# Kernel optimization log

Measured on AMD Instinct MI355X. Metric: run time of the kernel, lower is better.

Reference implementation:

```python
import jax, jax.numpy as jnp
import numpy as np

B, S, D, H, K = 2, 2048, 1024, 16, 64


def setup_inputs() -> dict:
    key = jax.random.key(0)
    k1, k2, k3 = jax.random.split(key, 3)
    x = jax.random.normal(k1, (B, S, D), dtype=jnp.float32)
    # causal mask: 1 where query can attend to key (key_pos <= pos)
    mask = jnp.tril(jnp.ones((S, S), dtype=jnp.float32))
    W_qkv = jax.random.normal(k2, (D, 3, H, K), dtype=jnp.float32) * 0.02
    b_qkv = jnp.zeros((3, H, K), dtype=jnp.float32)
    W_proj = jax.random.normal(k3, (H, K, D), dtype=jnp.float32) * 0.02
    b_proj = jnp.zeros((D,), dtype=jnp.float32)
    return {"x": x, "mask": mask, "W_qkv": W_qkv, "b_qkv": b_qkv,
            "W_proj": W_proj, "b_proj": b_proj, "layer_idx": 0}


def reference(x, mask, W_qkv, b_qkv, W_proj, b_proj, layer_idx):
    # c_attn: [B,S,D] @ [D,3,H,K] -> [B,S,3,H,K]
    qkv = jnp.einsum('bsd,dthk->bsthk', x, W_qkv) + b_qkv
    q, k, v = qkv[:, :, 0], qkv[:, :, 1], qkv[:, :, 2]  # each [B,S,H,K]
    scale = jax.lax.rsqrt(float(K))  # scale_attn_by_inverse_layer_idx=False
    q = q * scale
    # attn scores over key_size: [B,H,S(pos),S(key_pos)]
    scores = jnp.einsum('bshk,bthk->bhst', q, k)
    scores = scores + (1.0 - mask) * -1e9
    weights = jax.nn.softmax(scores, axis=-1).astype(x.dtype)
    # attn_pdrop = 0.0 -> dropout is identity
    attn_out = jnp.einsum('bhst,bthk->bshk', weights, v)  # [B,S,H,K]
    out = jnp.einsum('bshk,hkd->bsd', attn_out, W_proj) + b_proj
    return out
```

## Files before the change

### kernel.cpp

```cpp
#include <hip/hip_runtime.h>

typedef __bf16 bf16x8 __attribute__((ext_vector_type(8)));
typedef float f32x4 __attribute__((ext_vector_type(4)));
typedef float f32x16 __attribute__((ext_vector_type(16)));
typedef unsigned short u16x8 __attribute__((ext_vector_type(8)));

constexpr int S_LEN = 2048;
constexpr int QKV1  = 2 * 16 * 2048 * 64;

__device__ inline unsigned short f2bf(float f) {
    __bf16 h = (__bf16)f;
    return __builtin_bit_cast(unsigned short, h);
}

__device__ inline void gll16(const void* g, void* l) {
    __builtin_amdgcn_global_load_lds(
        (const __attribute__((address_space(1))) unsigned int*)g,
        (__attribute__((address_space(3))) unsigned int*)l,
        16, 0, 0);
}

__global__ __launch_bounds__(256) void cvt_f32_bf16(
    const float* __restrict__ src, unsigned short* __restrict__ dst, int n4)
{
    int i = blockIdx.x * 256 + threadIdx.x;
    if (i >= n4) return;
    float4 v = ((const float4*)src)[i];
    ushort4 u;
    u.x = f2bf(v.x); u.y = f2bf(v.y); u.z = f2bf(v.z); u.w = f2bf(v.w);
    ((ushort4*)dst)[i] = u;
}

__global__ __launch_bounds__(256) void transpose_cvt(
    const float* __restrict__ src, unsigned short* __restrict__ dst, int R, int C)
{
    __shared__ float t[32][33];
    const int c0 = blockIdx.x * 32, r0 = blockIdx.y * 32;
    const int tx = threadIdx.x, ty = threadIdx.y;
    #pragma unroll
    for (int i = 0; i < 4; ++i)
        t[ty * 4 + i][tx] = src[(size_t)(r0 + ty * 4 + i) * C + c0 + tx];
    __syncthreads();
    #pragma unroll
    for (int i = 0; i < 4; ++i)
        dst[(size_t)(c0 + ty * 4 + i) * R + r0 + tx] = f2bf(t[tx][ty * 4 + i]);
}

template<int EPI>
__global__ __launch_bounds__(256) void gemm128(
    const unsigned short* __restrict__ A,
    const unsigned short* __restrict__ Bt,
    const float* __restrict__ bias,
    void* __restrict__ outp, int M, int N, int K)
{
    __shared__ unsigned short As[2][128 * 32];
    __shared__ unsigned short Bs[2][128 * 32];
    const int tid = threadIdx.x, lane = tid & 63, wid = tid >> 6;
    const int q = lane & 15, g = lane >> 4;
    const int wr = wid >> 1, wc = wid & 1;

    const int nbx = N >> 7;
    const int cpx = gridDim.x >> 3;
    const int bid = blockIdx.x;
    const int swz = (bid & 7) * cpx + (bid >> 3);
    const int m0 = (swz / nbx) * 128, n0 = (swz % nbx) * 128;

    const int srow_in = lane >> 2;
    const int sslot   = (lane & 3) ^ (srow_in & 3);
    auto stage = [&](int buf, int k0) {
        #pragma unroll
        for (int i = 0; i < 2; ++i) {
            int c = wid * 2 + i;
            int row = c * 16 + srow_in;
            gll16(&A [(size_t)(m0 + row) * K + k0 + sslot * 8], &As[buf][c * 512]);
            gll16(&Bt[(size_t)(n0 + row) * K + k0 + sslot * 8], &Bs[buf][c * 512]);
        }
    };

    f32x4 acc[4][4];
    #pragma unroll
    for (int i = 0; i < 4; ++i)
        #pragma unroll
        for (int j = 0; j < 4; ++j) acc[i][j] = (f32x4){0.f, 0.f, 0.f, 0.f};

    const int NSTEP = K >> 5;
    const int rslot = (g ^ (q & 3)) * 8;
    stage(0, 0);
    __syncthreads();
    int cur = 0;

    for (int ks = 0; ks < NSTEP; ++ks) {
        if (ks + 1 < NSTEP) stage(cur ^ 1, (ks + 1) * 32);
        bf16x8 a[4], b[4];
        #pragma unroll
        for (int mi = 0; mi < 4; ++mi)
            a[mi] = *(const bf16x8*)&As[cur][(wr * 64 + mi * 16 + q) * 32 + rslot];
        #pragma unroll
        for (int ni = 0; ni < 4; ++ni)
            b[ni] = *(const bf16x8*)&Bs[cur][(wc * 64 + ni * 16 + q) * 32 + rslot];
        #pragma unroll
        for (int mi = 0; mi < 4; ++mi)
            #pragma unroll
            for (int ni = 0; ni < 4; ++ni)
                acc[mi][ni] = __builtin_amdgcn_mfma_f32_16x16x32_bf16(a[mi], b[ni], acc[mi][ni], 0, 0, 0);
        __syncthreads();
        cur ^= 1;
    }

    #pragma unroll
    for (int mi = 0; mi < 4; ++mi)
        #pragma unroll
        for (int ni = 0; ni < 4; ++ni)
            #pragma unroll
            for (int r = 0; r < 4; ++r) {
                int m = m0 + wr * 64 + mi * 16 + g * 4 + r;
                int n = n0 + wc * 64 + ni * 16 + q;
                float v = acc[mi][ni][r] + bias[n];
                if (EPI == 0) {
                    int t = n >> 10, rem = n & 1023;
                    if (t == 0) v *= 0.125f;
                    int h2 = rem >> 6, kk = rem & 63;
                    int bb = m >> 11, s = m & 2047;
                    size_t off;
                    if (t == 2)
                        off = 2 * (size_t)QKV1 + ((size_t)(bb * 16 + h2) * 64 + kk) * 2048 + s;
                    else
                        off = (size_t)t * QKV1 + ((size_t)(bb * 16 + h2) * 2048 + s) * 64 + kk;
                    ((unsigned short*)outp)[off] = f2bf(v);
                } else {
                    ((float*)outp)[(size_t)m * N + n] = v;
                }
            }
}

__global__ __launch_bounds__(256) void attn_fwd(
    const unsigned short* __restrict__ qkv,
    unsigned short* __restrict__ po, float2* __restrict__ pml)
{
    __shared__ unsigned short Ks[2][64][72];
    __shared__ unsigned short Vs[2][64][72];
    __shared__ float cLds[4][32];
    const int tid = threadIdx.x, lane = tid & 63, wid = tid >> 6;
    const int hi = lane >> 5, lq = lane & 31;
    const int bh = blockIdx.x;
    const int uy = (int)blockIdx.y;
    const int t    = 15 - (uy >> 1);
    const int half = uy & 1;
    const int jb0 = half ? (t + 1) : 0;
    const int jb1 = half ? (2 * t + 2) : (t + 1);
    const unsigned short* Qg = qkv + (size_t)bh * S_LEN * 64;
    const unsigned short* Kg = qkv + (size_t)QKV1 + (size_t)bh * S_LEN * 64;
    const unsigned short* Vt = qkv + 2 * (size_t)QKV1 + (size_t)bh * 64 * S_LEN;

    const int srr = tid >> 3, scc = (tid & 7) * 8;
    u16x8 kr[2], vr[2];
    auto stage_load = [&](int j0) {
        #pragma unroll
        for (int p = 0; p < 2; ++p) {
            kr[p] = *(const u16x8*)&Kg[(size_t)(j0 + srr + p * 32) * 64 + scc];
            vr[p] = *(const u16x8*)&Vt[(size_t)(srr + p * 32) * 2048 + j0 + scc];
        }
    };
    auto stage_write = [&](int b) {
        #pragma unroll
        for (int p = 0; p < 2; ++p) {
            *(u16x8*)&Ks[b][srr + p * 32][scc] = kr[p];
            *(u16x8*)&Vs[b][srr + p * 32][scc] = vr[p];
        }
    };

    const int qbase = t * 128 + wid * 32;
    const int qg = qbase + lq;

    bf16x8 qf[4];
    #pragma unroll
    for (int kc = 0; kc < 4; ++kc)
        qf[kc] = *(const bf16x8*)&Qg[(size_t)qg * 64 + kc * 16 + hi * 8];

    f32x16 z16;
    #pragma unroll
    for (int j = 0; j < 16; ++j) z16[j] = 0.f;

    f32x16 o0 = z16, o1 = z16;
    float m = -1e30f, lr = 0.f;

    stage_load(jb0 * 64);
    stage_write(0);
    int cur = 0;

    for (int jb = jb0; jb < jb1; ++jb) {
        const int j0 = jb * 64;
        if (jb + 1 < jb1) stage_load(j0 + 64);
        __syncthreads();

        if (j0 <= qbase + 31) {
            f32x16 s0, s1;
            __builtin_amdgcn_s_setprio(1);
            {
                bf16x8 k0 = *(const bf16x8*)&Ks[cur][lq][hi * 8];
                bf16x8 k1 = *(const bf16x8*)&Ks[cur][32 + lq][hi * 8];
                s0 = __builtin_amdgcn_mfma_f32_32x32x16_bf16(k0, qf[0], z16, 0, 0, 0);
                s1 = __builtin_amdgcn_mfma_f32_32x32x16_bf16(k1, qf[0], z16, 0, 0, 0);
            }
            #pragma unroll
            for (int kc = 1; kc < 4; ++kc) {
                bf16x8 k0 = *(const bf16x8*)&Ks[cur][lq][kc * 16 + hi * 8];
                bf16x8 k1 = *(const bf16x8*)&Ks[cur][32 + lq][kc * 16 + hi * 8];
                s0 = __builtin_amdgcn_mfma_f32_32x32x16_bf16(k0, qf[kc], s0, 0, 0, 0);
                s1 = __builtin_amdgcn_mfma_f32_32x32x16_bf16(k1, qf[kc], s1, 0, 0, 0);
            }
            __builtin_amdgcn_s_setprio(0);
            if (j0 + 63 > qbase) {
                #pragma unroll
                for (int r = 0; r < 16; ++r) {
                    int kv0 = j0 + (r & 3) + 8 * (r >> 2) + 4 * hi;
                    if (kv0 > qg)      s0[r] = -1e30f;
                    if (kv0 + 32 > qg) s1[r] = -1e30f;
                }
            }
            float tm[8];
            #pragma unroll
            for (int j = 0; j < 8; ++j)
                tm[j] = fmaxf(fmaxf(s0[j], s0[j + 8]), fmaxf(s1[j], s1[j + 8]));
            float pm_loc = fmaxf(fmaxf(fmaxf(tm[0], tm[1]), fmaxf(tm[2], tm[3])),
                                 fmaxf(fmaxf(tm[4], tm[5]), fmaxf(tm[6], tm[7])));
            if (!__all(pm_loc <= m + 8.0f)) {
                float pm = fmaxf(pm_loc, __shfl_xor(pm_loc, 32));
                float mn = fmaxf(m, pm);
                float corr = __expf(m - mn);
                m = mn; lr *= corr;
                if (lane < 32) cLds[wid][lq] = corr;
                #pragma unroll
                for (int r = 0; r < 16; ++r) {
                    float cq = cLds[wid][(r & 3) + 8 * (r >> 2) + 4 * hi];
                    o0[r] *= cq; o1[r] *= cq;
                }
            }
            float p0[16], p1[16], ts[16];
            #pragma unroll
            for (int j = 0; j < 16; ++j) {
                p0[j] = __expf(s0[j] - m);
                p1[j] = __expf(s1[j] - m);
                ts[j] = p0[j] + p1[j];
            }
            #pragma unroll
            for (int w = 8; w > 0; w >>= 1)
                #pragma unroll
                for (int j = 0; j < w; ++j) ts[j] += ts[j + w];
            lr += ts[0];
            int w0[8], w1[8];
            #pragma unroll
            for (int j = 0; j < 8; ++j) {
                asm("v_cvt_pk_bf16_f32 %0, %1, %2" : "=v"(w0[j]) : "v"(p0[2 * j]), "v"(p0[2 * j + 1]));
                asm("v_cvt_pk_bf16_f32 %0, %1, %2" : "=v"(w1[j]) : "v"(p1[2 * j]), "v"(p1[2 * j + 1]));
            }
            bf16x8 pa[4];
            auto mkfrag = [&](const int* w, int base) -> bf16x8 {
                int x0 = __shfl_xor(w[base + 0], 32);
                int x1 = __shfl_xor(w[base + 1], 32);
                int x2 = __shfl_xor(w[base + 2], 32);
                int x3 = __shfl_xor(w[base + 3], 32);
                int4 f;
                f.x = hi ? x2          : w[base + 0];
                f.y = hi ? x3          : w[base + 1];
                f.z = hi ? w[base + 2] : x0;
                f.w = hi ? w[base + 3] : x1;
                return __builtin_bit_cast(bf16x8, f);
            };
            pa[0] = mkfrag(w0, 0);
            pa[1] = mkfrag(w0, 4);
            pa[2] = mkfrag(w1, 0);
            pa[3] = mkfrag(w1, 4);
            __builtin_amdgcn_s_setprio(1);
            #pragma unroll
            for (int kc = 0; kc < 4; ++kc) {
                bf16x8 v0 = *(const bf16x8*)&Vs[cur][lq][kc * 16 + hi * 8];
                bf16x8 v1 = *(const bf16x8*)&Vs[cur][32 + lq][kc * 16 + hi * 8];
                o0 = __builtin_amdgcn_mfma_f32_32x32x16_bf16(pa[kc], v0, o0, 0, 0, 0);
                o1 = __builtin_amdgcn_mfma_f32_32x32x16_bf16(pa[kc], v1, o1, 0, 0, 0);
            }
            __builtin_amdgcn_s_setprio(0);
        }

        if (jb + 1 < jb1) stage_write(cur ^ 1);
        cur ^= 1;
    }

    const int unit = (bh * 16 + t) * 2 + half;
    float lr_full = lr + __shfl_xor(lr, 32);
    if (lane < 32) {
        float2 v; v.x = m; v.y = lr_full;
        pml[unit * 128 + wid * 32 + lq] = v;
    }
    #pragma unroll
    for (int r = 0; r < 16; ++r) {
        int lrow = wid * 32 + (r & 3) + 8 * (r >> 2) + 4 * hi;
        size_t off = ((size_t)unit * 128 + lrow) * 64;
        po[off + lq]      = f2bf(o0[r]);
        po[off + 32 + lq] = f2bf(o1[r]);
    }
}

__global__ __launch_bounds__(256) void attn_combine(
    const unsigned short* __restrict__ po, const float2* __restrict__ pml,
    unsigned short* __restrict__ aout)
{
    const int gid = blockIdx.x * 256 + threadIdx.x;
    const int row = gid >> 2;
    const int cg  = (gid & 3) * 16;
    const int bt = row >> 7, lrow = row & 127;
    const float2 ml0 = pml[(bt * 2 + 0) * 128 + lrow];
    const float2 ml1 = pml[(bt * 2 + 1) * 128 + lrow];
    const float ms = fmaxf(ml0.x, ml1.x);
    float w0 = __expf(ml0.x - ms), w1 = __expf(ml1.x - ms);
    const float inv = 1.0f / (ml0.y * w0 + ml1.y * w1);
    w0 *= inv; w1 *= inv;
    const size_t r0 = ((size_t)(bt * 2 + 0) * 128 + lrow) * 64 + cg;
    const size_t r1 = ((size_t)(bt * 2 + 1) * 128 + lrow) * 64 + cg;
    const int bh = bt >> 4, t = bt & 15;
    const int bb = bh >> 4, h = bh & 15;
    const int s = t * 128 + lrow;
    const size_t orow = ((size_t)(bb * 2048 + s)) * 1024 + h * 64 + cg;
    #pragma unroll
    for (int c = 0; c < 2; ++c) {
        u16x8 a = *(const u16x8*)&po[r0 + c * 8];
        u16x8 b = *(const u16x8*)&po[r1 + c * 8];
        u16x8 o;
        #pragma unroll
        for (int e = 0; e < 8; ++e) {
            float fa = __builtin_bit_cast(float, (unsigned)((unsigned short)a[e]) << 16);
            float fb = __builtin_bit_cast(float, (unsigned)((unsigned short)b[e]) << 16);
            o[e] = f2bf(fa * w0 + fb * w1);
        }
        *(u16x8*)&aout[orow + c * 8] = o;
    }
}

extern "C" void kernel_launch(void* const* d_in, const int* in_sizes, int n_in,
                              void* d_out, int out_size, void* d_ws, size_t ws_size,
                              hipStream_t stream) {
    const float* x     = (const float*)d_in[0];
    const float* Wqkv  = (const float*)d_in[2];
    const float* bqkv  = (const float*)d_in[3];
    const float* Wproj = (const float*)d_in[4];
    const float* bproj = (const float*)d_in[5];

    unsigned short* qkvb  = (unsigned short*)d_ws;
    unsigned short* aoutb = qkvb + 3 * (size_t)QKV1;
    float2*         pml   = (float2*)(aoutb + 4096 * 1024);
    unsigned short* Wt   = aoutb;
    unsigned short* Wt2  = qkvb;
    unsigned short* Xbf  = (unsigned short*)d_out;
    unsigned short* po   = (unsigned short*)d_out;

    cvt_f32_bf16<<<4096, 256, 0, stream>>>(x, Xbf, 4096 * 1024 / 4);
    transpose_cvt<<<dim3(96, 32), dim3(32, 8), 0, stream>>>(Wqkv, Wt, 1024, 3072);
    gemm128<0><<<768, 256, 0, stream>>>(Xbf, Wt, bqkv, qkvb, 4096, 3072, 1024);
    attn_fwd<<<dim3(32, 32), 256, 0, stream>>>(qkvb, po, pml);
    attn_combine<<<1024, 256, 0, stream>>>(po, pml, aoutb);
    transpose_cvt<<<dim3(32, 32), dim3(32, 8), 0, stream>>>(Wproj, Wt2, 1024, 1024);
    gemm128<1><<<256, 256, 0, stream>>>(aoutb, Wt2, bproj, d_out, 4096, 1024, 1024);
}
```

Baseline: 123.6 us.

## Replace QKV projection GEMM with 256x256-tile, 8-wave, double-buffered kernel

The QKV projection now runs on a new GEMM kernel that uses 256x256 output tiles, 512 threads (8 waves) and 128 KB of dynamic LDS. Each K step loads 64 columns through direct global-to-LDS loads, double-buffers them and interleaves the prefetch with MFMA phases using barriers and raised wave priority. The aim is more operand reuse per loaded byte and better overlap of loads with compute than the 128x128 kernel gave. The cost is only 192 workgroups on a 256-CU device, so some CUs sit idle and occupancy is lower. It also relies on tight hand-tuned waitcnt and barrier scheduling.

```diff
diff --git a/kernel.cpp b/kernel.cpp
--- a/kernel.cpp
+++ b/kernel.cpp
@@ -46,12 +46,154 @@
         dst[(size_t)(c0 + ty * 4 + i) * R + r0 + tx] = f2bf(t[tx][ty * 4 + i]);
 }
 
-template<int EPI>
-__global__ __launch_bounds__(256) void gemm128(
+__global__ __launch_bounds__(512) void gemm256(
     const unsigned short* __restrict__ A,
     const unsigned short* __restrict__ Bt,
     const float* __restrict__ bias,
-    void* __restrict__ outp, int M, int N, int K)
+    unsigned short* __restrict__ qkv, int M, int N, int K)
+{
+    extern __shared__ unsigned short lds[];
+    unsigned short* AsL = lds;
+    unsigned short* BsL = lds + 32768;
+    const int tid = threadIdx.x, lane = tid & 63, wid = tid >> 6;
+    const int q = lane & 15, g = lane >> 4;
+    const int wm = wid >> 2, wn = wid & 3;
+    const int nbx = N >> 8;
+    const int cpx = gridDim.x >> 3;
+    const int bid = blockIdx.x;
+    const int swz = (bid & 7) * cpx + (bid >> 3);
+    const int m0 = (swz / nbx) * 256, n0 = (swz % nbx) * 256;
+
+    const int rl = lane >> 2;
+    const int sl = (((lane & 3) ^ ((lane >> 3) & 3))) * 8;
+    auto stA = [&](int slot, int kh, int k0) {
+        const unsigned short* sp = &A[(size_t)(m0 + wid * 32 + rl) * K + k0 + kh * 32 + sl];
+        unsigned short* d = &AsL[((slot * 2 + kh) * 256 + wid * 32) * 32];
+        gll16(sp, d);
+        gll16(sp + (size_t)16 * K, d + 16 * 32);
+    };
+    auto stB = [&](int slot, int kh, int k0) {
+        const unsigned short* sp = &Bt[(size_t)(n0 + wid * 32 + rl) * K + k0 + kh * 32 + sl];
+        unsigned short* d = &BsL[((slot * 2 + kh) * 256 + wid * 32) * 32];
+        gll16(sp, d);
+        gll16(sp + (size_t)16 * K, d + 16 * 32);
+    };
+
+    f32x4 acc[8][4];
+    #pragma unroll
+    for (int i = 0; i < 8; ++i)
+        #pragma unroll
+        for (int j = 0; j < 4; ++j) acc[i][j] = (f32x4){0.f, 0.f, 0.f, 0.f};
+
+    const int kq = (q >> 1) & 3;
+    const int rcol = (g ^ kq) * 8;
+    const int NSTEP = K >> 6;
+
+    stA(0, 0, 0); stB(0, 0, 0); stA(0, 1, 0); stB(0, 1, 0);
+    asm volatile("s_waitcnt vmcnt(4)" ::: "memory");
+    __builtin_amdgcn_s_barrier();
+    __builtin_amdgcn_sched_barrier(0);
+
+    for (int j = 0; j < NSTEP; ++j) {
+        const int s = j & 1;
+        const bool pf = (j + 1 < NSTEP);
+        const int kn = (j + 1) * 64;
+        const size_t abase = (size_t)(s * 2) * 8192;
+        const size_t abase1 = abase + 8192;
+        bf16x8 a[4], b[4];
+        #pragma unroll
+        for (int ni = 0; ni < 4; ++ni)
+            b[ni] = *(const bf16x8*)&BsL[abase + (size_t)(wn * 64 + ni * 16 + q) * 32 + rcol];
+        #pragma unroll
+        for (int mi = 0; mi < 4; ++mi)
+            a[mi] = *(const bf16x8*)&AsL[abase + (size_t)(wm * 128 + mi * 16 + q) * 32 + rcol];
+        if (pf) stA(s ^ 1, 0, kn);
+        __builtin_amdgcn_s_barrier();
+        __builtin_amdgcn_s_setprio(1);
+        #pragma unroll
+        for (int mi = 0; mi < 4; ++mi)
+            #pragma unroll
+            for (int ni = 0; ni < 4; ++ni)
+                acc[mi][ni] = __builtin_amdgcn_mfma_f32_16x16x32_bf16(a[mi], b[ni], acc[mi][ni], 0, 0, 0);
+        __builtin_amdgcn_s_setprio(0);
+        __builtin_amdgcn_s_barrier();
+        #pragma unroll
+        for (int mi = 0; mi < 4; ++mi)
+            a[mi] = *(const bf16x8*)&AsL[abase + (size_t)(wm * 128 + (mi + 4) * 16 + q) * 32 + rcol];
+        if (pf) stB(s ^ 1, 0, kn);
+        __builtin_amdgcn_s_barrier();
+        __builtin_amdgcn_s_setprio(1);
+        #pragma unroll
+        for (int mi = 0; mi < 4; ++mi)
+            #pragma unroll
+            for (int ni = 0; ni < 4; ++ni)
+                acc[mi + 4][ni] = __builtin_amdgcn_mfma_f32_16x16x32_bf16(a[mi], b[ni], acc[mi + 4][ni], 0, 0, 0);
+        __builtin_amdgcn_s_setprio(0);
+        if (pf) asm volatile("s_waitcnt vmcnt(4)" ::: "memory");
+        else    asm volatile("s_waitcnt vmcnt(0)" ::: "memory");
+        __builtin_amdgcn_s_barrier();
+        __builtin_amdgcn_sched_barrier(0);
+        #pragma unroll
+        for (int ni = 0; ni < 4; ++ni)
+            b[ni] = *(const bf16x8*)&BsL[abase1 + (size_t)(wn * 64 + ni * 16 + q) * 32 + rcol];
+        #pragma unroll
+        for (int mi = 0; mi < 4; ++mi)
+            a[mi] = *(const bf16x8*)&AsL[abase1 + (size_t)(wm * 128 + mi * 16 + q) * 32 + rcol];
+        if (pf) stA(s ^ 1, 1, kn);
+        __builtin_amdgcn_s_barrier();
+        __builtin_amdgcn_s_setprio(1);
+        #pragma unroll
+        for (int mi = 0; mi < 4; ++mi)
+            #pragma unroll
+            for (int ni = 0; ni < 4; ++ni)
+                acc[mi][ni] = __builtin_amdgcn_mfma_f32_16x16x32_bf16(a[mi], b[ni], acc[mi][ni], 0, 0, 0);
+        __builtin_amdgcn_s_setprio(0);
+        __builtin_amdgcn_s_barrier();
+        #pragma unroll
+        for (int mi = 0; mi < 4; ++mi)
+            a[mi] = *(const bf16x8*)&AsL[abase1 + (size_t)(wm * 128 + (mi + 4) * 16 + q) * 32 + rcol];
+        if (pf) stB(s ^ 1, 1, kn);
+        __builtin_amdgcn_s_barrier();
+        __builtin_amdgcn_s_setprio(1);
+        #pragma unroll
+        for (int mi = 0; mi < 4; ++mi)
+            #pragma unroll
+            for (int ni = 0; ni < 4; ++ni)
+                acc[mi + 4][ni] = __builtin_amdgcn_mfma_f32_16x16x32_bf16(a[mi], b[ni], acc[mi + 4][ni], 0, 0, 0);
+        __builtin_amdgcn_s_setprio(0);
+        if (pf) {
+            asm volatile("s_waitcnt vmcnt(4)" ::: "memory");
+            __builtin_amdgcn_s_barrier();
+            __builtin_amdgcn_sched_barrier(0);
+        }
+    }
+
+    #pragma unroll
+    for (int mi = 0; mi < 8; ++mi)
+        #pragma unroll
+        for (int ni = 0; ni < 4; ++ni)
+            #pragma unroll
+            for (int r = 0; r < 4; ++r) {
+                int m = m0 + wm * 128 + mi * 16 + g * 4 + r;
+                int n = n0 + wn * 64 + ni * 16 + q;
+                float v = acc[mi][ni][r] + bias[n];
+                int t = n >> 10, rem = n & 1023;
+                if (t == 0) v *= 0.125f;
+                int h2 = rem >> 6, kk = rem & 63;
+                int bb = m >> 11, s2 = m & 2047;
+                size_t off;
+                if (t == 2)
+                    off = 2 * (size_t)QKV1 + ((size_t)(bb * 16 + h2) * 64 + kk) * 2048 + s2;
+                else
+                    off = (size_t)t * QKV1 + ((size_t)(bb * 16 + h2) * 2048 + s2) * 64 + kk;
+                qkv[off] = f2bf(v);
+            }
+}
+
+template<int EPI>
+__global__ __launch_bounds__(256) void gemm128(
+    const unsigned short* __restrict__ A, const unsigned short* __restrict__ Bt,
+    const float* __restrict__ bias, void* __restrict__ outp, int M, int N, int K)
 {
     __shared__ unsigned short As[2][128 * 32];
     __shared__ unsigned short Bs[2][128 * 32];
@@ -353,9 +495,12 @@
     unsigned short* Xbf  = (unsigned short*)d_out;
     unsigned short* po   = (unsigned short*)d_out;
 
+    (void)hipFuncSetAttribute((const void*)gemm256,
+                              hipFuncAttributeMaxDynamicSharedMemorySize, 131072);
+
     cvt_f32_bf16<<<4096, 256, 0, stream>>>(x, Xbf, 4096 * 1024 / 4);
     transpose_cvt<<<dim3(96, 32), dim3(32, 8), 0, stream>>>(Wqkv, Wt, 1024, 3072);
-    gemm128<0><<<768, 256, 0, stream>>>(Xbf, Wt, bqkv, qkvb, 4096, 3072, 1024);
+    gemm256<<<192, 512, 131072, stream>>>(Xbf, Wt, bqkv, qkvb, 4096, 3072, 1024);
     attn_fwd<<<dim3(32, 32), 256, 0, stream>>>(qkvb, po, pml);
     attn_combine<<<1024, 256, 0, stream>>>(po, pml, aoutb);
     transpose_cvt<<<dim3(32, 32), dim3(32, 8), 0, stream>>>(Wproj, Wt2, 1024, 1024);
```

Measured after the change: 142.8 us. +15.6%, slower.
